# Kernel optimization log

Measured on AMD Instinct MI355X. Metric: run time of the kernel, lower is better.

Reference implementation:

```python
import jax, jax.numpy as jnp
import numpy as np

N_NODES = 100000


def setup_inputs() -> dict:
    key = jax.random.key(0)
    ks = jax.random.split(key, 6)
    F_IN, F_CH, F_OUT = 64, 64, 64
    E = 1200000
    x = jax.random.normal(ks[0], (N_NODES, F_IN), dtype=jnp.float32)
    edge_index = jax.random.randint(ks[1], (2, E), 0, N_NODES, dtype=jnp.int64)
    # MLP params (PyTorch Linear default init scale ~ 1/sqrt(fan_in))
    s1 = 1.0 / np.sqrt(2 * F_IN)
    s2 = 1.0 / np.sqrt(F_CH)
    W1 = jax.random.uniform(ks[2], (2 * F_IN, F_CH), jnp.float32, -s1, s1)
    b1 = jax.random.uniform(ks[3], (F_CH,), jnp.float32, -s1, s1)
    W2 = jax.random.uniform(ks[4], (F_CH, F_OUT), jnp.float32, -s2, s2)
    b2 = jax.random.uniform(ks[5], (F_OUT,), jnp.float32, -s2, s2)
    return {"x": x, "edge_index": edge_index, "W1": W1, "b1": b1, "W2": W2, "b2": b2}


def reference(x, edge_index, W1, b1, W2, b2):
    # PyG EdgeConv with aggr='add': out_i = sum_j MLP(concat[x_i, x_j - x_i])
    src = edge_index[0]  # j (source / neighbor)
    dst = edge_index[1]  # i (target, aggregation index)
    x_i = x[dst]                     # [E, F]
    x_j = x[src]                     # [E, F]
    msg = jnp.concatenate([x_i, x_j - x_i], axis=-1)      # [E, 2F]
    h = jax.nn.relu(msg @ W1 + b1) @ W2 + b2               # [E, F_out]
    agg = jax.ops.segment_sum(h, dst, num_segments=N_NODES)  # [N, F_out]
    return jnp.tanh(agg)
```

## Files before the change

kernel.cpp:

```cpp
#include <hip/hip_runtime.h>
#include <math.h>


#define FDIM 64
#define BN 128
#define BSH 7
#define CAPB 2048
#define MAXB 1024
#define EPB 4096
#define XS_W 33
#define PRE_SMEM 24832

typedef unsigned int u32;
typedef unsigned short u16;
typedef _Float16 hf;

__device__ __forceinline__ float bf_lo(u32 u) {
    union { u32 i; float f; } c; c.i = u << 16; return c.f;
}
__device__ __forceinline__ float bf_hi(u32 u) {
    union { u32 i; float f; } c; c.i = u & 0xffff0000u; return c.f;
}
__device__ __forceinline__ u32 f2bf_rne(float f) {
    union { float f; u32 u; } c; c.f = f;
    u32 u = c.u;
    u += 0x7fffu + ((u >> 16) & 1u);
    return u >> 16;
}
__device__ __forceinline__ u32 f2h(float f) {
    union { u16 s; hf h; } c; c.h = (hf)f; return (u32)c.s;
}
__device__ __forceinline__ float h_lo(u32 u) {
    union { u16 s; hf h; } c; c.s = (u16)(u & 0xffffu); return (float)c.h;
}
__device__ __forceinline__ float h_hi(u32 u) {
    union { u16 s; hf h; } c; c.s = (u16)(u >> 16); return (float)c.h;
}

__global__ __launch_bounds__(256) void wprep_k(
    const float* __restrict__ W1, const float* __restrict__ W2,
    u32* __restrict__ Wchg, u32* __restrict__ W2hg)
{
    const int tid = threadIdx.x;
    for (int i = tid; i < 4096; i += 256) {
        int k = i >> 6, p = i & 63;
        u32 pk;
        if (p < 32) {
            int c = p * 2;
            float a0 = W1[k * 64 + c]     - W1[(64 + k) * 64 + c];
            float a1 = W1[k * 64 + c + 1] - W1[(64 + k) * 64 + c + 1];
            pk = f2h(a0) | (f2h(a1) << 16);
        } else {
            int c = (p - 32) * 2;
            pk = f2h(W1[(64 + k) * 64 + c]) | (f2h(W1[(64 + k) * 64 + c + 1]) << 16);
        }
        Wchg[i] = pk;
    }
    for (int i = tid; i < 2048; i += 256) {
        int k = i >> 5, c2 = i & 31;
        W2hg[i] = f2h(W2[k * 64 + c2 * 2]) | (f2h(W2[k * 64 + c2 * 2 + 1]) << 16);
    }
}

__global__ __launch_bounds__(256) void prep_k(
    const float* __restrict__ x, const u32* __restrict__ Wchg,
    const float* __restrict__ b1, u16* __restrict__ Ah,
    u16* __restrict__ Bmh, const int* __restrict__ ei,
    u32* __restrict__ slotB, int* __restrict__ gcnt,
    int N, int E, int NB, int nPre, int nBin)
{
    __shared__ __align__(16) char smem[PRE_SMEM];
    const int idx = blockIdx.x;
    const int tid = threadIdx.x;

    if ((idx % 6) == 5) {
        const int bb = idx / 6;
        if (bb >= nBin) return;
        int* histL = (int*)smem;
        int* gbase = histL + MAXB;
        const int e0 = bb * EPB;

        for (int j = tid; j < NB; j += 256) histL[j] = 0;
        __syncthreads();

        #pragma unroll
        for (int i = 0; i < EPB / 256; ++i) {
            int e = e0 + i * 256 + tid;
            if (e < E) {
                int d = ei[E + e];
                atomicAdd(&histL[d >> BSH], 1);
            }
        }
        __syncthreads();

        for (int j = tid; j < NB; j += 256) {
            int h = histL[j];
            gbase[j] = (h > 0) ? atomicAdd(&gcnt[j], h) : 0;
            histL[j] = 0;
        }
        __syncthreads();

        #pragma unroll
        for (int i = 0; i < EPB / 256; ++i) {
            int e = e0 + i * 256 + tid;
            if (e < E) {
                int s = ei[e];
                int d = ei[E + e];
                int b = d >> BSH;
                int pos = gbase[b] + atomicAdd(&histL[b], 1);
                if (pos < CAPB)
                    slotB[(size_t)b * CAPB + pos] =
                        ((u32)(d & (BN - 1)) << 20) | (u32)s;
            }
        }
        return;
    }

    const int pb = idx - idx / 6;
    if (pb >= nPre) return;
    u32 (*Wch)[64] = (u32(*)[64])smem;
    u32* xs = (u32*)(smem + 16384);

    const int node0 = pb * 64;

    {
        const uint4* Wg4 = (const uint4*)Wchg;
        #pragma unroll
        for (int it = 0; it < 4; ++it) {
            int i = it * 256 + tid;
            uint4 w = Wg4[i];
            *(uint4*)&Wch[i >> 4][(i & 15) * 4] = w;
        }
    }
    {
        const float4* X4 = (const float4*)x;
        #pragma unroll
        for (int it = 0; it < 4; ++it) {
            int i = it * 256 + tid;
            int n = i >> 4, k4 = i & 15;
            int gn = node0 + n;
            float4 v = make_float4(0.f, 0.f, 0.f, 0.f);
            if (gn < N) v = X4[(size_t)gn * 16 + k4];
            xs[n * XS_W + 2 * k4]     = f2h(v.x) | (f2h(v.y) << 16);
            xs[n * XS_W + 2 * k4 + 1] = f2h(v.z) | (f2h(v.w) << 16);
        }
    }
    __syncthreads();

    const int ng = tid & 15, cg = tid >> 4;
    const int n0 = ng * 4, c0 = cg * 8;
    const int wbase = (cg & 7) * 4 + ((cg >> 3) * 32);

    float acc[4][8];
    #pragma unroll
    for (int ci = 0; ci < 8; ++ci) {
        float init = b1[(c0 + ci) & 63];
        if (c0 >= 64) init = 0.f;
        #pragma unroll
        for (int ni = 0; ni < 4; ++ni) acc[ni][ci] = init;
    }

    #pragma unroll 4
    for (int kk = 0; kk < 32; ++kk) {
        u32 xv[4];
        #pragma unroll
        for (int ni = 0; ni < 4; ++ni) xv[ni] = xs[(n0 + ni) * XS_W + kk];
        uint4 w0 = *(const uint4*)&Wch[2 * kk][wbase];
        uint4 w1 = *(const uint4*)&Wch[2 * kk + 1][wbase];
        float ws0[8] = {h_lo(w0.x), h_hi(w0.x), h_lo(w0.y), h_hi(w0.y),
                        h_lo(w0.z), h_hi(w0.z), h_lo(w0.w), h_hi(w0.w)};
        float ws1[8] = {h_lo(w1.x), h_hi(w1.x), h_lo(w1.y), h_hi(w1.y),
                        h_lo(w1.z), h_hi(w1.z), h_lo(w1.w), h_hi(w1.w)};
        #pragma unroll
        for (int ni = 0; ni < 4; ++ni) {
            float xa = h_lo(xv[ni]);
            float xb = h_hi(xv[ni]);
            #pragma unroll
            for (int ci = 0; ci < 8; ++ci)
                acc[ni][ci] += xa * ws0[ci] + xb * ws1[ci];
        }
    }

    #pragma unroll
    for (int ni = 0; ni < 4; ++ni) {
        int n = node0 + n0 + ni;
        if (n >= N) break;
        if (c0 < 64) {
            uint4 pk;
            pk.x = f2h(acc[ni][0]) | (f2h(acc[ni][1]) << 16);
            pk.y = f2h(acc[ni][2]) | (f2h(acc[ni][3]) << 16);
            pk.z = f2h(acc[ni][4]) | (f2h(acc[ni][5]) << 16);
            pk.w = f2h(acc[ni][6]) | (f2h(acc[ni][7]) << 16);
            *(uint4*)&Ah[(size_t)n * 64 + c0] = pk;
        } else {
            uint4 pk;
            pk.x = f2bf_rne(acc[ni][0]) | (f2bf_rne(acc[ni][1]) << 16);
            pk.y = f2bf_rne(acc[ni][2]) | (f2bf_rne(acc[ni][3]) << 16);
            pk.z = f2bf_rne(acc[ni][4]) | (f2bf_rne(acc[ni][5]) << 16);
            pk.w = f2bf_rne(acc[ni][6]) | (f2bf_rne(acc[ni][7]) << 16);
            *(uint4*)&Bmh[(size_t)n * 64 + (c0 - 64)] = pk;
        }
    }
}

__device__ __forceinline__ float4 relu4add(float4 acc, float4 a, float4 b) {
    acc.x += fmaxf(a.x + b.x, 0.f);
    acc.y += fmaxf(a.y + b.y, 0.f);
    acc.z += fmaxf(a.z + b.z, 0.f);
    acc.w += fmaxf(a.w + b.w, 0.f);
    return acc;
}
__device__ __forceinline__ float4 relu4add_m(float4 acc, float4 a, float4 b, bool m) {
    acc.x += m ? fmaxf(a.x + b.x, 0.f) : 0.f;
    acc.y += m ? fmaxf(a.y + b.y, 0.f) : 0.f;
    acc.z += m ? fmaxf(a.z + b.z, 0.f) : 0.f;
    acc.w += m ? fmaxf(a.w + b.w, 0.f) : 0.f;
    return acc;
}
__device__ __forceinline__ float4 bf4(uint2 u) {
    return make_float4(bf_lo(u.x), bf_hi(u.x), bf_lo(u.y), bf_hi(u.y));
}

__global__ __launch_bounds__(256) void fused_agg(
    const u16* __restrict__ Ah, const u16* __restrict__ Bmh,
    const u32* __restrict__ slotB, const int* __restrict__ gcnt,
    const u32* __restrict__ W2hg, const float* __restrict__ b2,
    float* __restrict__ out, int N)
{
    __shared__ __align__(16) u32 W2h[64][34];
    __shared__ __align__(16) u32 pool[BN * 17 * 2];
    __shared__ u32 csrS[CAPB];
    __shared__ int histL[BN];
    __shared__ int rowO[BN + 1];
    __shared__ int ofs[BN];
    __shared__ float b2s[64];

    u32* eStage = pool;
    uint2* aggTb = (uint2*)pool;

    const int tid = threadIdx.x;
    const int b = blockIdx.x;
    const int node0 = b * BN;
    const int cntB = min(gcnt[b], CAPB);

    {
        const uint4* Wg4 = (const uint4*)W2hg;
        #pragma unroll
        for (int it = 0; it < 2; ++it) {
            int i = it * 256 + tid;
            uint4 w = Wg4[i];
            *(uint4*)&W2h[i >> 3][(i & 7) * 4] = w;
        }
    }
    if (tid < 64) b2s[tid] = b2[tid];
    if (tid < BN) histL[tid] = 0;
    __syncthreads();

    for (int i = tid; i < cntB; i += 256) {
        u32 e = slotB[(size_t)b * CAPB + i];
        eStage[i] = e;
        atomicAdd(&histL[e >> 20], 1);
    }
    __syncthreads();

    if (tid < 64) {
        int l = tid;
        int h0 = histL[2 * l], h1 = histL[2 * l + 1];
        int s = h0 + h1, inc = s;
        #pragma unroll
        for (int off = 1; off < 64; off <<= 1) {
            int t = __shfl_up(inc, off);
            if (l >= off) inc += t;
        }
        int base = inc - s;
        rowO[2 * l] = base; rowO[2 * l + 1] = base + h0;
        ofs[2 * l] = base;  ofs[2 * l + 1] = base + h0;
        if (l == 63) rowO[BN] = inc;
    }
    __syncthreads();

    for (int i = tid; i < cntB; i += 256) {
        u32 e = eStage[i];
        int pos = atomicAdd(&ofs[e >> 20], 1);
        csrS[pos] = e & 0xFFFFFu;
    }
    __syncthreads();

    {
        const int q = tid & 15, ng = tid >> 4;
        const uint2* __restrict__ B2 = (const uint2*)Bmh;
        const uint2* __restrict__ A2 = (const uint2*)Ah;
        #pragma unroll
        for (int h = 0; h < 8; ++h) {
            int nl = ng + h * 16;
            int gn = node0 + nl;
            int start = rowO[nl];
            int d = (gn < N) ? (rowO[nl + 1] - start) : 0;
            float4 a = make_float4(0.f, 0.f, 0.f, 0.f);
            if (gn < N) {
                uint2 ua = A2[(size_t)gn * 16 + q];
                a = make_float4(h_lo(ua.x), h_hi(ua.x), h_lo(ua.y), h_hi(ua.y));
            }
            float4 acc = make_float4(0.f, 0.f, 0.f, 0.f);

            int j = 0;
            for (; j + 8 <= d; j += 8) {
                int ss[8];
                uint2 bb[8];
                #pragma unroll
                for (int t = 0; t < 8; ++t) ss[t] = csrS[start + j + t];
                #pragma unroll
                for (int t = 0; t < 8; ++t) bb[t] = B2[(size_t)ss[t] * 16 + q];
                #pragma unroll
                for (int t = 0; t < 8; ++t) acc = relu4add(acc, a, bf4(bb[t]));
            }
            if (j < d) {
                int ss[8];
                uint2 bb[8];
                #pragma unroll
                for (int t = 0; t < 8; ++t) ss[t] = csrS[start + min(j + t, d - 1)];
                #pragma unroll
                for (int t = 0; t < 8; ++t) bb[t] = B2[(size_t)ss[t] * 16 + q];
                acc = relu4add(acc, a, bf4(bb[0]));
                #pragma unroll
                for (int t = 1; t < 8; ++t)
                    acc = relu4add_m(acc, a, bf4(bb[t]), j + t < d);
            }
            uint2 pk;
            pk.x = f2h(acc.x) | (f2h(acc.y) << 16);
            pk.y = f2h(acc.z) | (f2h(acc.w) << 16);
            aggTb[nl * 17 + q] = pk;
        }
    }
    __syncthreads();

    {
        const int cg = tid & 15, g0 = tid >> 4;
        const int c0 = cg * 4;
        #pragma unroll
        for (int h = 0; h < 2; ++h) {
            int g = g0 + h * 16;
            int nb0 = g * 4;
            float o[4][4];
            #pragma unroll
            for (int ni = 0; ni < 4; ++ni) {
                float dg = (float)(rowO[nb0 + ni + 1] - rowO[nb0 + ni]);
                #pragma unroll
                for (int ci = 0; ci < 4; ++ci) o[ni][ci] = dg * b2s[c0 + ci];
            }
            #pragma unroll 2
            for (int kc = 0; kc < 16; ++kc) {
                uint2 u0 = aggTb[(nb0 + 0) * 17 + kc];
                uint2 u1 = aggTb[(nb0 + 1) * 17 + kc];
                uint2 u2 = aggTb[(nb0 + 2) * 17 + kc];
                uint2 u3 = aggTb[(nb0 + 3) * 17 + kc];
                #pragma unroll
                for (int kk = 0; kk < 4; ++kk) {
                    uint2 w2p = *(const uint2*)&W2h[kc * 4 + kk][cg * 2];
                    float wv[4] = {h_lo(w2p.x), h_hi(w2p.x), h_lo(w2p.y), h_hi(w2p.y)};
                    float a0 = (kk < 2) ? ((kk == 0) ? h_lo(u0.x) : h_hi(u0.x))
                                        : ((kk == 2) ? h_lo(u0.y) : h_hi(u0.y));
                    float a1 = (kk < 2) ? ((kk == 0) ? h_lo(u1.x) : h_hi(u1.x))
                                        : ((kk == 2) ? h_lo(u1.y) : h_hi(u1.y));
                    float a2 = (kk < 2) ? ((kk == 0) ? h_lo(u2.x) : h_hi(u2.x))
                                        : ((kk == 2) ? h_lo(u2.y) : h_hi(u2.y));
                    float a3 = (kk < 2) ? ((kk == 0) ? h_lo(u3.x) : h_hi(u3.x))
                                        : ((kk == 2) ? h_lo(u3.y) : h_hi(u3.y));
                    #pragma unroll
                    for (int ci = 0; ci < 4; ++ci) {
                        o[0][ci] += a0 * wv[ci];
                        o[1][ci] += a1 * wv[ci];
                        o[2][ci] += a2 * wv[ci];
                        o[3][ci] += a3 * wv[ci];
                    }
                }
            }
            #pragma unroll
            for (int ni = 0; ni < 4; ++ni) {
                int gn = node0 + nb0 + ni;
                if (gn < N) {
                    float4 r = make_float4(tanhf(o[ni][0]), tanhf(o[ni][1]),
                                           tanhf(o[ni][2]), tanhf(o[ni][3]));
                    ((float4*)out)[(size_t)gn * 16 + cg] = r;
                }
            }
        }
    }
}

extern "C" void kernel_launch(void* const* d_in, const int* in_sizes, int n_in,
                              void* d_out, int out_size, void* d_ws, size_t ws_size,
                              hipStream_t stream)
{
    const float* x  = (const float*)d_in[0];
    const int*   ei = (const int*)d_in[1];
    const float* W1 = (const float*)d_in[2];
    const float* b1 = (const float*)d_in[3];
    const float* W2 = (const float*)d_in[4];
    const float* b2 = (const float*)d_in[5];
    float* out = (float*)d_out;

    const int N = in_sizes[0] / FDIM;
    const int E = in_sizes[1] / 2;
    const int NB = (N + BN - 1) / BN;

    u16*   Ah    = (u16*)d_ws;
    u16*   Bmh   = Ah + (size_t)N * FDIM;
    u32*   slotB = (u32*)(Bmh + (size_t)N * FDIM);
    u32*   Wchg  = slotB + (size_t)NB * CAPB;
    u32*   W2hg  = Wchg + 4096;
    int*   gcnt  = (int*)(W2hg + 2048);

    hipMemsetAsync(gcnt, 0, (size_t)NB * sizeof(int), stream);

    wprep_k<<<1, 256, 0, stream>>>(W1, W2, Wchg, W2hg);

    const int nPre = (N + 63) / 64;
    const int nBin = (E + EPB - 1) / EPB;
    int T = (nPre * 6 + 4) / 5;
    while (T - T / 6 < nPre) ++T;
    if (T < 6 * nBin) T = 6 * nBin;

    prep_k<<<T, 256, 0, stream>>>(x, Wchg, b1, Ah, Bmh, ei, slotB, gcnt,
                                  N, E, NB, nPre, nBin);
    fused_agg<<<NB, 256, 0, stream>>>(Ah, Bmh, slotB, gcnt, W2hg, b2, out, N);
}
```

Measured before the change: 195.3 us.

## Replace block-local histogram binning with direct padded global atomics per edge

The edge binning path no longer builds a shared-memory histogram and reserves ranges with one global atomic per bin. Each edge now does a global atomicAdd on a per-bucket counter, with counters padded to 16 ints so they sit in separate cache lines. The counter zeroing moves from a memset into the weight-prep kernel, which removes one launch. This cuts three syncthreads phases and the shared-memory loops over all buckets, but it raises global atomic traffic from about one per bucket per block to one per edge, and contention grows since roughly 100 edges land in each bucket.

```diff
diff --git a/kernel.cpp b/kernel.cpp
--- a/kernel.cpp
+++ b/kernel.cpp
@@ -6,10 +6,10 @@
 #define BN 128
 #define BSH 7
 #define CAPB 2048
-#define MAXB 1024
 #define EPB 4096
 #define XS_W 33
 #define PRE_SMEM 24832
+#define GPAD 16
 
 typedef unsigned int u32;
 typedef unsigned short u16;
@@ -39,7 +39,8 @@
 
 __global__ __launch_bounds__(256) void wprep_k(
     const float* __restrict__ W1, const float* __restrict__ W2,
-    u32* __restrict__ Wchg, u32* __restrict__ W2hg)
+    u32* __restrict__ Wchg, u32* __restrict__ W2hg,
+    int* __restrict__ gcntP, int NB)
 {
     const int tid = threadIdx.x;
     for (int i = tid; i < 4096; i += 256) {
@@ -60,13 +61,14 @@
         int k = i >> 5, c2 = i & 31;
         W2hg[i] = f2h(W2[k * 64 + c2 * 2]) | (f2h(W2[k * 64 + c2 * 2 + 1]) << 16);
     }
+    for (int i = tid; i < NB * GPAD; i += 256) gcntP[i] = 0;
 }
 
 __global__ __launch_bounds__(256) void prep_k(
     const float* __restrict__ x, const u32* __restrict__ Wchg,
     const float* __restrict__ b1, u16* __restrict__ Ah,
     u16* __restrict__ Bmh, const int* __restrict__ ei,
-    u32* __restrict__ slotB, int* __restrict__ gcnt,
+    u32* __restrict__ slotB, int* __restrict__ gcntP,
     int N, int E, int NB, int nPre, int nBin)
 {
     __shared__ __align__(16) char smem[PRE_SMEM];
@@ -76,41 +78,28 @@
     if ((idx % 6) == 5) {
         const int bb = idx / 6;
         if (bb >= nBin) return;
-        int* histL = (int*)smem;
-        int* gbase = histL + MAXB;
         const int e0 = bb * EPB;
-
-        for (int j = tid; j < NB; j += 256) histL[j] = 0;
-        __syncthreads();
-
-        #pragma unroll
-        for (int i = 0; i < EPB / 256; ++i) {
-            int e = e0 + i * 256 + tid;
-            if (e < E) {
-                int d = ei[E + e];
-                atomicAdd(&histL[d >> BSH], 1);
-            }
-        }
-        __syncthreads();
-
-        for (int j = tid; j < NB; j += 256) {
-            int h = histL[j];
-            gbase[j] = (h > 0) ? atomicAdd(&gcnt[j], h) : 0;
-            histL[j] = 0;
-        }
-        __syncthreads();
-
-        #pragma unroll
-        for (int i = 0; i < EPB / 256; ++i) {
-            int e = e0 + i * 256 + tid;
-            if (e < E) {
-                int s = ei[e];
-                int d = ei[E + e];
-                int b = d >> BSH;
-                int pos = gbase[b] + atomicAdd(&histL[b], 1);
-                if (pos < CAPB)
-                    slotB[(size_t)b * CAPB + pos] =
-                        ((u32)(d & (BN - 1)) << 20) | (u32)s;
+        #pragma unroll 2
+        for (int half = 0; half < 2; ++half) {
+            int sv[8], dv[8], pv[8];
+            #pragma unroll
+            for (int i = 0; i < 8; ++i) {
+                int e = e0 + (half * 8 + i) * 256 + tid;
+                bool ok = e < E;
+                sv[i] = ok ? ei[e] : 0;
+                dv[i] = ok ? ei[E + e] : -1;
+            }
+            #pragma unroll
+            for (int i = 0; i < 8; ++i)
+                pv[i] = (dv[i] >= 0) ? atomicAdd(&gcntP[(dv[i] >> BSH) * GPAD], 1)
+                                     : CAPB;
+            #pragma unroll
+            for (int i = 0; i < 8; ++i) {
+                if (dv[i] >= 0 && pv[i] < CAPB) {
+                    int b = dv[i] >> BSH;
+                    slotB[(size_t)b * CAPB + pv[i]] =
+                        ((u32)(dv[i] & (BN - 1)) << 20) | (u32)sv[i];
+                }
             }
         }
         return;
@@ -223,7 +212,7 @@
 
 __global__ __launch_bounds__(256) void fused_agg(
     const u16* __restrict__ Ah, const u16* __restrict__ Bmh,
-    const u32* __restrict__ slotB, const int* __restrict__ gcnt,
+    const u32* __restrict__ slotB, const int* __restrict__ gcntP,
     const u32* __restrict__ W2hg, const float* __restrict__ b2,
     float* __restrict__ out, int N)
 {
@@ -241,7 +230,7 @@
     const int tid = threadIdx.x;
     const int b = blockIdx.x;
     const int node0 = b * BN;
-    const int cntB = min(gcnt[b], CAPB);
+    const int cntB = min(gcntP[b * GPAD], CAPB);
 
     {
         const uint4* Wg4 = (const uint4*)W2hg;
@@ -409,11 +398,9 @@
     u32*   slotB = (u32*)(Bmh + (size_t)N * FDIM);
     u32*   Wchg  = slotB + (size_t)NB * CAPB;
     u32*   W2hg  = Wchg + 4096;
-    int*   gcnt  = (int*)(W2hg + 2048);
-
-    hipMemsetAsync(gcnt, 0, (size_t)NB * sizeof(int), stream);
-
-    wprep_k<<<1, 256, 0, stream>>>(W1, W2, Wchg, W2hg);
+    int*   gcntP = (int*)(W2hg + 2048);
+
+    wprep_k<<<1, 256, 0, stream>>>(W1, W2, Wchg, W2hg, gcntP, NB);
 
     const int nPre = (N + 63) / 64;
     const int nBin = (E + EPB - 1) / EPB;
@@ -421,7 +408,7 @@
     while (T - T / 6 < nPre) ++T;
     if (T < 6 * nBin) T = 6 * nBin;
 
-    prep_k<<<T, 256, 0, stream>>>(x, Wchg, b1, Ah, Bmh, ei, slotB, gcnt,
+    prep_k<<<T, 256, 0, stream>>>(x, Wchg, b1, Ah, Bmh, ei, slotB, gcntP,
                                   N, E, NB, nPre, nBin);
-    fused_agg<<<NB, 256, 0, stream>>>(Ah, Bmh, slotB, gcnt, W2hg, b2, out, N);
-}
+    fused_agg<<<NB, 256, 0, stream>>>(Ah, Bmh, slotB, gcntP, W2hg, b2, out, N);
+}
```

Result: slower. 231.2 us (+18.4%).
